# Performance work log

Hardware: AMD Instinct MI355X
Metric: run time of the kernel (lower is better)

## Reference

```python
import jax, jax.numpy as jnp
import numpy as np

ALPHA = 100.0   # norse SuperSpike surrogate-gradient sharpness (default)
DT = 0.001      # norse LIFBoxParameters default dt

@jax.custom_vjp
def heaviside(x):
    # spike function with SuperSpike surrogate gradient (norse method='super')
    return (x > 0).astype(x.dtype)

def _hs_fwd(x):
    return (x > 0).astype(x.dtype), x

def _hs_bwd(x, g):
    return (g / (ALPHA * jnp.abs(x) + 1.0) ** 2,)

heaviside.defvjp(_hs_fwd, _hs_bwd)


def setup_inputs() -> dict:
    key = jax.random.key(0)
    k0, k1, k2, k3, k4 = jax.random.split(key, 5)
    B, F, T = 256, 10, 8192
    inputs = jax.random.normal(k0, (B, F, T), dtype=jnp.float32)
    # learned scalar LIF parameters (one per parallel temporal layer)
    tau = jnp.array([200.0, 300.0, 600.0], dtype=jnp.float32)   # tau_mem_inv
    v_th = jnp.array([0.006, 0.008, 0.013], dtype=jnp.float32)  # thresholds
    conv_w = jax.random.normal(k1, (1, 3, 1, 1), dtype=jnp.float32) * 0.5
    conv_b = jax.random.normal(k2, (1,), dtype=jnp.float32) * 0.1
    lin_w = jax.random.normal(k3, (2, 10), dtype=jnp.float32) * 0.3
    lin_b = jax.random.normal(k4, (2,), dtype=jnp.float32) * 0.1
    return {"inputs": inputs, "tau": tau, "v_th": v_th,
            "conv_w": conv_w, "conv_b": conv_b, "lin_w": lin_w, "lin_b": lin_b}


def reference(inputs, tau, v_th, conv_w, conv_b, lin_w, lin_b):
    # inputs: [B, F, T]
    B, F, T = inputs.shape
    x_t = jnp.transpose(inputs, (2, 0, 1))          # [T, B, F], time-major
    tau3 = tau[:, None, None]                        # [3,1,1] broadcast over B,F
    vth3 = v_th[:, None, None]
    v0 = jnp.zeros((3, B, F), dtype=inputs.dtype)    # v_leak = 0 initial state

    def step(v, x):
        # LIFBox dynamics: dv = dt * tau_inv * (v_leak - v + i), v_leak=v_reset=0
        v = v + DT * tau3 * (x[None, :, :] - v)      # [3,B,F]
        z = heaviside(v - vth3)                      # spikes
        v = (1.0 - z) * v                            # reset to v_reset=0 on spike
        return v, z

    _, zs = jax.lax.scan(step, v0, x_t)              # zs: [T, 3, B, F]
    resp = jnp.transpose(zs, (2, 1, 3, 0))           # [B, 3, F, T]

    # 1x1 Conv2d over the 3 LIF channels -> [B, F, T]
    conv = jnp.einsum('bcft,c->bft', resp, conv_w[0, :, 0, 0]) + conv_b[0]
    # Linear over feature dim F=10 -> 2, output [B, 2, T]
    out = jnp.einsum('bft,of->bot', conv, lin_w) + lin_b[None, :, None]
    return out
```

## Files before the change

### kernel.cpp

```cpp
#include <hip/hip_runtime.h>


#define T_LEN 8192
#define NF 10
#define NSEQ 30
#define CHUNK 256
#define WARM 128
#define NCHUNKS 32
#define NWIN 12
#define WWIN 4
#define NROW 20
#define BUF4 (NROW * 8)

__device__ __forceinline__ float lif_step(float xx, float v, float k, float vt, bool& s) {
  float d  = __fsub_rn(xx, v);
  float p  = __fmul_rn(k, d);
  float vn = __fadd_rn(v, p);
  s = vn > vt;
  return s ? 0.0f : vn;
}

__device__ __forceinline__ float lut_sum(unsigned m, const float* lut, int o, float bias) {
  float acc = bias;
#pragma unroll
  for (int g = 0; g < 6; ++g) {
    unsigned val = (m >> (5 * g)) & 31u;
    acc += lut[(g * 2 + o) * 32 + val];
  }
  return acc;
}

__global__ __launch_bounds__(64, 4) void lif_chunked(
    const float* __restrict__ x,
    const float* __restrict__ tau,
    const float* __restrict__ vth,
    const float* __restrict__ convw,
    const float* __restrict__ convb,
    const float* __restrict__ linw,
    const float* __restrict__ linb,
    float* __restrict__ out)
{
  const int b    = blockIdx.x;
  const int cb   = blockIdx.y;
  const int lane = threadIdx.x;
  const int half = lane >> 5;
  const int j    = lane & 31;
  const bool active = j < NSEQ;
  const int c = active ? j / NF : 0;
  const int f = active ? j % NF : 0;

  __shared__ float lut[384];
  __shared__ float4 xbuf[2][BUF4];
#pragma unroll
  for (int e = 0; e < 6; ++e) {
    int id = lane + 64 * e;
    int g = id >> 6, rem = id & 63, oo = rem >> 5, val = rem & 31;
    float sacc = 0.0f;
#pragma unroll
    for (int p = 0; p < 5; ++p) {
      if (val & (1 << p)) {
        int jj = 5 * g + p;
        sacc += convw[jj / NF] * linw[oo * NF + (jj % NF)];
      }
    }
    lut[id] = sacc;
  }
  __syncthreads();

  const float k  = __fmul_rn(0.001f, tau[c]);
  const float vt = active ? vth[c] : 3.0e38f;
  const int chunk = cb * 2 + half;

  const int srow = half * NF + f;
  const int sw   = srow & 7;
  const float4* rbase = &xbuf[0][srow * 8];

  const float4* gp[3];
  float4*       lp[3];
  int           adj[3];
#pragma unroll
  for (int i = 0; i < 3; ++i) {
    int id  = (i == 0) ? lane : (i == 1) ? (lane + 64) : ((lane & 31) + 128);
    int row = id >> 3;
    int q   = id & 7;
    int h   = row / NF;
    int fr  = row % NF;
    int ch  = 2 * cb + h;
    int ts  = (ch == 0) ? 0 : ch * CHUNK - WARM;
    gp[i]  = (const float4*)(x + ((size_t)b * NF + fr) * (size_t)T_LEN + ts) + q;
    lp[i]  = &xbuf[0][row * 8 + (q ^ (row & 7))];
    adj[i] = (ch == 0) ? -(WARM / 4) : 0;
  }

  const int o  = half;
  const int tt = j;
  float wsum = 0.0f;
#pragma unroll
  for (int f2 = 0; f2 < NF; ++f2) wsum += linw[o * NF + f2];
  const float bias = linb[o] + convb[0] * wsum;

  const int tA = 2 * cb * CHUNK;
  float* outA = out + ((size_t)b * 2 + o) * T_LEN + tA;
  float* outB = outA + CHUNK;

  {
    float4 s0 = gp[0][0], s1 = gp[1][0], s2 = gp[2][0];
    *lp[0] = s0; *lp[1] = s1; *lp[2] = s2;
    gp[0] += 8; gp[1] += 8; gp[2] += 8;
  }

  float v = 0.0f;

#pragma unroll 1
  for (int w = 0; w < NWIN; ++w) {
    const bool haveNext = (w + 1 < NWIN);
    float4 s0, s1, s2;
    if (haveNext) {
      if (w + 1 == WWIN) {
        gp[0] += adj[0]; gp[1] += adj[1]; gp[2] += adj[2];
      }
      s0 = gp[0][0]; s1 = gp[1][0]; s2 = gp[2][0];
      gp[0] += 8; gp[1] += 8; gp[2] += 8;
    }

    const float4* rp = rbase + (w & 1) * BUF4;

    if (w < WWIN) {
      float4 x0 = rp[0 ^ sw];
      float4 x1 = rp[1 ^ sw];
#pragma unroll
      for (int q = 0; q < 8; ++q) {
        float4 xn = x1;
        if (q + 2 < 8) xn = rp[(q + 2) ^ sw];
        bool s;
        v = lif_step(x0.x, v, k, vt, s);
        v = lif_step(x0.y, v, k, vt, s);
        v = lif_step(x0.z, v, k, vt, s);
        v = lif_step(x0.w, v, k, vt, s);
        x0 = x1; x1 = xn;
      }
      if (w == WWIN - 1) v = (chunk == 0) ? 0.0f : v;
    } else {
      unsigned mA = 0, mB = 0;
      float4 x0 = rp[0 ^ sw];
      float4 x1 = rp[1 ^ sw];
#pragma unroll
      for (int q = 0; q < 8; ++q) {
        float4 xn = x1;
        if (q + 2 < 8) xn = rp[(q + 2) ^ sw];
        float xs[4] = {x0.x, x0.y, x0.z, x0.w};
#pragma unroll
        for (int r = 0; r < 4; ++r) {
          bool s;
          v = lif_step(xs[r], v, k, vt, s);
          unsigned long long ub = __ballot(s);
          const int t = q * 4 + r;
          if (tt == t) {
            mA = (unsigned)(ub & 0xffffffffull);
            mB = (unsigned)(ub >> 32);
          }
        }
        x0 = x1; x1 = xn;
      }
      const int ow = w - WWIN;
      outA[ow * 32 + tt] = lut_sum(mA, lut, o, bias);
      outB[ow * 32 + tt] = lut_sum(mB, lut, o, bias);
    }

    if (haveNext) {
      const int nb = (w + 1) & 1;
      *(lp[0] + nb * BUF4) = s0;
      *(lp[1] + nb * BUF4) = s1;
      *(lp[2] + nb * BUF4) = s2;
    }
  }
}

extern "C" void kernel_launch(void* const* d_in, const int* in_sizes, int n_in,
                              void* d_out, int out_size, void* d_ws, size_t ws_size,
                              hipStream_t stream) {
  const float* x     = (const float*)d_in[0];
  const float* tau   = (const float*)d_in[1];
  const float* vthp  = (const float*)d_in[2];
  const float* convw = (const float*)d_in[3];
  const float* convb = (const float*)d_in[4];
  const float* linw  = (const float*)d_in[5];
  const float* linb  = (const float*)d_in[6];
  float* out = (float*)d_out;

  const int B = in_sizes[0] / (NF * T_LEN);
  lif_chunked<<<dim3(B, NCHUNKS / 2), dim3(64), 0, stream>>>(
      x, tau, vthp, convw, convb, linw, linb, out);
}
```

Baseline: 148.6 us.

## Deepen global prefetch to two windows ahead with triple-buffered LDS

Global loads for the input window are now issued two windows ahead and held in registers, with LDS grown from double to triple buffering so the store for window w+1 happens while loads for w+2 are in flight. The warmup and output branches are merged into one loop body that always does the ballot capture, which removes divergent code paths but adds ballot work during warmup windows. It also replaces pointer arrays with scalar variables to help register allocation. This costs more registers and LDS, and the kernel has no __syncthreads between LDS writes and reads, relying on a single 64-lane wavefront.

After: 151.5 us. No clear change (+2.0%).

```diff
diff --git a/kernel.cpp b/kernel.cpp
--- a/kernel.cpp
+++ b/kernel.cpp
@@ -30,6 +30,17 @@
   return acc;
 }
 
+#define STEP_CAP(XX, T)                                            \
+  {                                                                \
+    bool s;                                                        \
+    v = lif_step((XX), v, k, vt, s);                               \
+    unsigned long long ub = __ballot(s);                           \
+    if (tt == (T)) {                                               \
+      mA = (unsigned)(ub & 0xffffffffull);                         \
+      mB = (unsigned)(ub >> 32);                                   \
+    }                                                              \
+  }
+
 __global__ __launch_bounds__(64, 4) void lif_chunked(
     const float* __restrict__ x,
     const float* __restrict__ tau,
@@ -50,7 +61,7 @@
   const int f = active ? j % NF : 0;
 
   __shared__ float lut[384];
-  __shared__ float4 xbuf[2][BUF4];
+  __shared__ float4 xbuf[3][BUF4];
 #pragma unroll
   for (int e = 0; e < 6; ++e) {
     int id = lane + 64 * e;
@@ -73,24 +84,24 @@
 
   const int srow = half * NF + f;
   const int sw   = srow & 7;
-  const float4* rbase = &xbuf[0][srow * 8];
 
-  const float4* gp[3];
-  float4*       lp[3];
-  int           adj[3];
-#pragma unroll
-  for (int i = 0; i < 3; ++i) {
-    int id  = (i == 0) ? lane : (i == 1) ? (lane + 64) : ((lane & 31) + 128);
-    int row = id >> 3;
-    int q   = id & 7;
-    int h   = row / NF;
-    int fr  = row % NF;
-    int ch  = 2 * cb + h;
-    int ts  = (ch == 0) ? 0 : ch * CHUNK - WARM;
-    gp[i]  = (const float4*)(x + ((size_t)b * NF + fr) * (size_t)T_LEN + ts) + q;
-    lp[i]  = &xbuf[0][row * 8 + (q ^ (row & 7))];
-    adj[i] = (ch == 0) ? -(WARM / 4) : 0;
-  }
+  const int id0 = lane,        id1 = lane + 64,  id2 = (lane & 31) + 128;
+  const int row0 = id0 >> 3,   row1 = id1 >> 3,  row2 = id2 >> 3;
+  const int q0 = id0 & 7,      q1 = id1 & 7,     q2 = id2 & 7;
+  const int ch0 = 2 * cb + row0 / NF, ch1 = 2 * cb + row1 / NF, ch2 = 2 * cb + row2 / NF;
+  const int fr0 = row0 % NF,   fr1 = row1 % NF,  fr2 = row2 % NF;
+  const int ts0 = (ch0 == 0) ? 0 : ch0 * CHUNK - WARM;
+  const int ts1 = (ch1 == 0) ? 0 : ch1 * CHUNK - WARM;
+  const int ts2 = (ch2 == 0) ? 0 : ch2 * CHUNK - WARM;
+  const float4* gp0 = (const float4*)(x + ((size_t)b * NF + fr0) * (size_t)T_LEN + ts0) + q0;
+  const float4* gp1 = (const float4*)(x + ((size_t)b * NF + fr1) * (size_t)T_LEN + ts1) + q1;
+  const float4* gp2 = (const float4*)(x + ((size_t)b * NF + fr2) * (size_t)T_LEN + ts2) + q2;
+  const int lpo0 = row0 * 8 + (q0 ^ (row0 & 7));
+  const int lpo1 = row1 * 8 + (q1 ^ (row1 & 7));
+  const int lpo2 = row2 * 8 + (q2 ^ (row2 & 7));
+  const int adj0 = (ch0 == 0) ? -(WARM / 4) : 0;
+  const int adj1 = (ch1 == 0) ? -(WARM / 4) : 0;
+  const int adj2 = (ch2 == 0) ? -(WARM / 4) : 0;
 
   const int o  = half;
   const int tt = j;
@@ -103,76 +114,54 @@
   float* outA = out + ((size_t)b * 2 + o) * T_LEN + tA;
   float* outB = outA + CHUNK;
 
+  float4 rA0 = gp0[0], rA1 = gp1[0], rA2 = gp2[0];
+  gp0 += 8; gp1 += 8; gp2 += 8;
   {
-    float4 s0 = gp[0][0], s1 = gp[1][0], s2 = gp[2][0];
-    *lp[0] = s0; *lp[1] = s1; *lp[2] = s2;
-    gp[0] += 8; gp[1] += 8; gp[2] += 8;
+    float4* wp = &xbuf[0][0];
+    wp[lpo0] = rA0; wp[lpo1] = rA1; wp[lpo2] = rA2;
   }
+  rA0 = gp0[0]; rA1 = gp1[0]; rA2 = gp2[0];
+  gp0 += 8; gp1 += 8; gp2 += 8;
 
   float v = 0.0f;
 
 #pragma unroll 1
   for (int w = 0; w < NWIN; ++w) {
-    const bool haveNext = (w + 1 < NWIN);
-    float4 s0, s1, s2;
-    if (haveNext) {
-      if (w + 1 == WWIN) {
-        gp[0] += adj[0]; gp[1] += adj[1]; gp[2] += adj[2];
-      }
-      s0 = gp[0][0]; s1 = gp[1][0]; s2 = gp[2][0];
-      gp[0] += 8; gp[1] += 8; gp[2] += 8;
+    float4 rB0, rB1, rB2;
+    const bool issueNext = (w + 2 < NWIN);
+    if (issueNext) {
+      if (w + 2 == WWIN) { gp0 += adj0; gp1 += adj1; gp2 += adj2; }
+      rB0 = gp0[0]; rB1 = gp1[0]; rB2 = gp2[0];
+      gp0 += 8; gp1 += 8; gp2 += 8;
     }
 
-    const float4* rp = rbase + (w & 1) * BUF4;
+    const float4* rp = &xbuf[w % 3][srow * 8];
+    unsigned mA = 0, mB = 0;
+    float4 x0 = rp[0 ^ sw];
+    float4 x1 = rp[1 ^ sw];
+#pragma unroll
+    for (int q = 0; q < 8; ++q) {
+      float4 xn = x1;
+      if (q + 2 < 8) xn = rp[(q + 2) ^ sw];
+      STEP_CAP(x0.x, 4 * q + 0)
+      STEP_CAP(x0.y, 4 * q + 1)
+      STEP_CAP(x0.z, 4 * q + 2)
+      STEP_CAP(x0.w, 4 * q + 3)
+      x0 = x1; x1 = xn;
+    }
 
-    if (w < WWIN) {
-      float4 x0 = rp[0 ^ sw];
-      float4 x1 = rp[1 ^ sw];
-#pragma unroll
-      for (int q = 0; q < 8; ++q) {
-        float4 xn = x1;
-        if (q + 2 < 8) xn = rp[(q + 2) ^ sw];
-        bool s;
-        v = lif_step(x0.x, v, k, vt, s);
-        v = lif_step(x0.y, v, k, vt, s);
-        v = lif_step(x0.z, v, k, vt, s);
-        v = lif_step(x0.w, v, k, vt, s);
-        x0 = x1; x1 = xn;
-      }
-      if (w == WWIN - 1) v = (chunk == 0) ? 0.0f : v;
-    } else {
-      unsigned mA = 0, mB = 0;
-      float4 x0 = rp[0 ^ sw];
-      float4 x1 = rp[1 ^ sw];
-#pragma unroll
-      for (int q = 0; q < 8; ++q) {
-        float4 xn = x1;
-        if (q + 2 < 8) xn = rp[(q + 2) ^ sw];
-        float xs[4] = {x0.x, x0.y, x0.z, x0.w};
-#pragma unroll
-        for (int r = 0; r < 4; ++r) {
-          bool s;
-          v = lif_step(xs[r], v, k, vt, s);
-          unsigned long long ub = __ballot(s);
-          const int t = q * 4 + r;
-          if (tt == t) {
-            mA = (unsigned)(ub & 0xffffffffull);
-            mB = (unsigned)(ub >> 32);
-          }
-        }
-        x0 = x1; x1 = xn;
-      }
+    if (w >= WWIN) {
       const int ow = w - WWIN;
       outA[ow * 32 + tt] = lut_sum(mA, lut, o, bias);
       outB[ow * 32 + tt] = lut_sum(mB, lut, o, bias);
     }
+    if (w == WWIN - 1) v = (chunk == 0) ? 0.0f : v;
 
-    if (haveNext) {
-      const int nb = (w + 1) & 1;
-      *(lp[0] + nb * BUF4) = s0;
-      *(lp[1] + nb * BUF4) = s1;
-      *(lp[2] + nb * BUF4) = s2;
+    if (w + 1 < NWIN) {
+      float4* wp = &xbuf[(w + 1) % 3][0];
+      wp[lpo0] = rA0; wp[lpo1] = rA1; wp[lpo2] = rA2;
     }
+    rA0 = rB0; rA1 = rB1; rA2 = rB2;
   }
 }
 
```
